# Kernel optimization log

Hardware: AMD Instinct MI355X
Metric: run time of the kernel (lower is better)

The kernel has to match this reference:

```python
import jax, jax.numpy as jnp
import numpy as np

N = 30000      # input points
M = 7500       # sampled queries = floor(N * ratio), ratio=0.25
K = 16         # neighbors per query
D_X = 64       # input feature dim
D_REL = 64     # point_pos_nn output dim
D_F = D_X + D_REL  # fij_hat dim = 128


def setup_inputs() -> dict:
    key = jax.random.key(0)
    ks = jax.random.split(key, 6)
    x = jax.random.normal(ks[0], (N, D_X), jnp.float32)
    pos = jax.random.normal(ks[1], (N, 3), jnp.float32)
    idx = jax.random.randint(ks[2], (M,), 0, N)
    W_pos = jax.random.normal(ks[3], (10, D_REL), jnp.float32) / jnp.sqrt(10.0)
    b_pos = jnp.zeros((D_REL,), jnp.float32)
    W_att = jax.random.normal(ks[4], (D_F, D_F), jnp.float32) / jnp.sqrt(float(D_F))
    b_att = jnp.zeros((D_F,), jnp.float32)
    W_glob = jax.random.normal(ks[5], (D_F, D_F), jnp.float32) / jnp.sqrt(float(D_F))
    b_glob = jnp.zeros((D_F,), jnp.float32)
    return {"x": x, "pos": pos, "idx": idx, "W_pos": W_pos, "b_pos": b_pos,
            "W_att": W_att, "b_att": b_att, "W_glob": W_glob, "b_glob": b_glob}


def reference(x, pos, idx, W_pos, b_pos, W_att, b_att, W_glob, b_glob):
    # --- KNN: brute-force squared distances from sampled queries to all points ---
    pos_q = pos[idx]                                         # [M, 3]
    d2 = ((pos_q * pos_q).sum(-1)[:, None]
          + (pos * pos).sum(-1)[None, :]
          - 2.0 * pos_q @ pos.T)                             # [M, N]
    _, nbr = jax.lax.top_k(-d2, K)                           # [M, K] neighbor indices

    # --- Local Spatial Encoding (message) ---
    pos_j = pos[nbr]                                         # [M, K, 3]
    pos_i = jnp.broadcast_to(pos_q[:, None, :], pos_j.shape) # [M, K, 3]
    vij = pos_i - pos_j                                      # [M, K, 3]
    dij = jnp.linalg.norm(vij, axis=-1, keepdims=True)       # [M, K, 1]
    rel = jnp.concatenate([pos_i, pos_j, vij, dij], axis=-1) # [M, K, 10]
    rij = jax.nn.relu(rel @ W_pos + b_pos)                   # [M, K, D_REL]

    # --- Attentive pooling ---
    fij = jnp.concatenate([x[nbr], rij], axis=-1)            # [M, K, D_F]
    g = fij @ W_att + b_att                                  # [M, K, D_F]
    s = jax.nn.softmax(g, axis=-1)                           # softmax over feature dim
    aggr = jnp.mean(s * fij, axis=1)                         # mean over K neighbors -> [M, D_F]

    # --- global_nn (update) ---
    return jax.nn.relu(aggr @ W_glob + b_glob)               # [M, D_F]
```

## Files before the change

kernel.cpp:

```cpp
#include <hip/hip_runtime.h>
#include <stdint.h>

#define KNB     16
#define GD      64
#define GTOT    (GD * GD * GD)
#define GORIG   (-6.5f)
#define GEDGE   0.203125f
#define GINV    (1.0f / GEDGE)
#define CAPW    640
#define PROBE_T 48

typedef short short8 __attribute__((ext_vector_type(8)));
typedef float floatx4 __attribute__((ext_vector_type(4)));

__device__ __forceinline__ unsigned short f2bf(float x) {
  union { float f; uint32_t u; } v; v.f = x;
  uint32_t u = v.u + 0x7FFFu + ((v.u >> 16) & 1u);
  return (unsigned short)(u >> 16);
}
__device__ __forceinline__ float bf2f(unsigned short b) {
  return __uint_as_float(((uint32_t)b) << 16);
}
__device__ __forceinline__ int cellco(float v) {
  int c = (int)floorf((v - GORIG) * GINV);
  return c < 0 ? 0 : (c > GD - 1 ? GD - 1 : c);
}

__global__ void zero_kernel(int* __restrict__ count) {
  int i = (blockIdx.x * 256 + threadIdx.x) * 4;
  *(int4*)(count + i) = make_int4(0, 0, 0, 0);
}

__global__ void prep_kernel(const float* __restrict__ x,
                            const float* __restrict__ pos,
                            const float* __restrict__ W_att,
                            unsigned short* __restrict__ xb,
                            float4* __restrict__ pos4,
                            unsigned short* __restrict__ Wt,
                            int* __restrict__ ptcell,
                            int* __restrict__ count, int N) {
  int id = blockIdx.x * 256 + threadIdx.x;
  int nx8 = N * 8;
  if (id < nx8) {
    const float4* src = (const float4*)x + (size_t)id * 2;
    float4 a = src[0], b = src[1];
    short8 v;
    v[0] = (short)f2bf(a.x); v[1] = (short)f2bf(a.y);
    v[2] = (short)f2bf(a.z); v[3] = (short)f2bf(a.w);
    v[4] = (short)f2bf(b.x); v[5] = (short)f2bf(b.y);
    v[6] = (short)f2bf(b.z); v[7] = (short)f2bf(b.w);
    *(short8*)(xb + (size_t)id * 8) = v;
  } else if (id < nx8 + N) {
    int j = id - nx8;
    float px = pos[3 * j], py = pos[3 * j + 1], pz = pos[3 * j + 2];
    float pp = fmaf(px, px, fmaf(py, py, pz * pz));
    pos4[j] = make_float4(px, py, pz, pp);
    int cid = (cellco(pz) * GD + cellco(py)) * GD + cellco(px);
    ptcell[j] = cid;
    atomicAdd(&count[cid], 1);
  } else if (id < nx8 + N + 128 * 128) {
    int t = id - nx8 - N;
    int c = t >> 7, f = t & 127;
    Wt[f * 128 + c] = f2bf(W_att[t]);
  }
}

__global__ __launch_bounds__(256) void vscan_x(const int* __restrict__ count,
                                               int* __restrict__ V) {
  int row = blockIdx.x * 4 + (threadIdx.x >> 6);
  int ln = threadIdx.x & 63;
  int i = row * GD + ln;
  int v = count[i];
#pragma unroll
  for (int off = 1; off < 64; off <<= 1) {
    int y = __shfl_up(v, off);
    if (ln >= off) v += y;
  }
  V[i] = v;
}

__global__ __launch_bounds__(256) void vscan_y(int* __restrict__ V) {
  int pair = blockIdx.x * 4 + (threadIdx.x >> 6);
  int z = pair >> 6, x = pair & 63;
  int ln = threadIdx.x & 63;
  int i = (z * GD + ln) * GD + x;
  int v = V[i];
#pragma unroll
  for (int off = 1; off < 64; off <<= 1) {
    int y = __shfl_up(v, off);
    if (ln >= off) v += y;
  }
  V[i] = v;
}

__global__ __launch_bounds__(256) void vscan_z(int* __restrict__ V) {
  int pair = blockIdx.x * 4 + (threadIdx.x >> 6);
  int ln = threadIdx.x & 63;
  int i = ln * GD * GD + pair;
  int v = V[i];
#pragma unroll
  for (int off = 1; off < 64; off <<= 1) {
    int y = __shfl_up(v, off);
    if (ln >= off) v += y;
  }
  V[i] = v;
}

__global__ __launch_bounds__(256) void derive_kernel(
    const int* __restrict__ V, int* __restrict__ cell_start,
    int* __restrict__ cursor) {
  int cid = blockIdx.x * 256 + threadIdx.x;
  int x = cid & 63, y = (cid >> 6) & 63, z = cid >> 12;
  int s = 0;
  if (z > 0) s += V[((z - 1) * GD + 63) * GD + 63];
  if (y > 0) {
    s += V[(z * GD + (y - 1)) * GD + 63];
    if (z > 0) s -= V[((z - 1) * GD + (y - 1)) * GD + 63];
  }
  if (x > 0) {
    s += V[(z * GD + y) * GD + (x - 1)];
    if (y > 0) s -= V[(z * GD + (y - 1)) * GD + (x - 1)];
    if (z > 0) s -= V[((z - 1) * GD + y) * GD + (x - 1)];
    if (z > 0 && y > 0) s += V[((z - 1) * GD + (y - 1)) * GD + (x - 1)];
  }
  cell_start[cid] = s;
  cursor[cid] = s;
  if (cid == 0) cell_start[GTOT] = V[GTOT - 1];
}

__global__ void scatter_kernel(const float4* __restrict__ pos4,
                               const int* __restrict__ ptcell,
                               int* __restrict__ cursor,
                               float4* __restrict__ spos4,
                               int* __restrict__ sid, int N) {
  int j = blockIdx.x * 256 + threadIdx.x;
  if (j >= N) return;
  int cid = ptcell[j];
  int slot = atomicAdd(&cursor[cid], 1);
  spos4[slot] = pos4[j];
  sid[slot] = j;
}

__device__ __forceinline__ unsigned long long top16_reg(
    unsigned long long* candw, int tot, int ln) {
  unsigned long long c[CAPW / 64];
#pragma unroll
  for (int chk = 0; chk < CAPW / 64; ++chk) {
    int slot = chk * 64 + ln;
    c[chk] = (slot < tot) ? candw[slot] : ~0ull;
  }
  unsigned long long mykey = ~0ull, last = 0;
#pragma unroll
  for (int r = 0; r < KNB; ++r) {
    unsigned long long mn = c[0];
#pragma unroll
    for (int chk = 1; chk < CAPW / 64; ++chk) mn = (c[chk] < mn) ? c[chk] : mn;
#pragma unroll
    for (int off = 1; off < 64; off <<= 1) {
      unsigned long long o = __shfl_xor(mn, off);
      mn = (o < mn) ? o : mn;
    }
    if (ln == r) mykey = mn;
    last = mn;
#pragma unroll
    for (int chk = 0; chk < CAPW / 64; ++chk)
      if (c[chk] == mn) c[chk] = ~0ull;
  }
  if (ln < KNB) candw[ln] = mykey;
  return last;
}

__device__ __forceinline__ void drain_annulus(
    const float4* __restrict__ spos4, const int* __restrict__ sid,
    const int* __restrict__ cell_start, unsigned long long* candw,
    float4 qp, int cqx, int cqy, int cqz, int slo, int shi, int ln,
    int& tot, unsigned long long& taukey) {
  const int z0 = (cqz - shi < 0) ? 0 : cqz - shi;
  const int z1 = (cqz + shi > GD - 1) ? GD - 1 : cqz + shi;
  const int y0 = (cqy - shi < 0) ? 0 : cqy - shi;
  const int y1 = (cqy + shi > GD - 1) ? GD - 1 : cqy + shi;
  const int wy = y1 - y0 + 1;
  const int npair = (z1 - z0 + 1) * wy;
  for (int base = 0; base < npair; base += 64) {
    int i = base + ln;
    int stA = 0, lA = 0, stB = 0, lB = 0;
    if (i < npair) {
      int zz = z0 + i / wy;
      int yy = y0 + (i - (i / wy) * wy);
      int dz = zz - cqz, dy = yy - cqy;
      int az = dz < 0 ? -dz : dz, ay = dy < 0 ? -dy : dy;
      int ch = az > ay ? az : ay;
      int rowbase = (zz * GD + yy) * GD;
      if (ch > slo) {
        int x0 = cqx - shi; if (x0 < 0) x0 = 0;
        int x1 = cqx + shi; if (x1 > GD - 1) x1 = GD - 1;
        stA = cell_start[rowbase + x0];
        lA  = cell_start[rowbase + x1 + 1] - stA;
      } else {
        int xl0 = cqx - shi; if (xl0 < 0) xl0 = 0;
        int xl1 = cqx - slo - 1;
        if (xl1 >= xl0) {
          stA = cell_start[rowbase + xl0];
          lA  = cell_start[rowbase + xl1 + 1] - stA;
        }
        int xr0 = cqx + slo + 1;
        int xr1 = cqx + shi; if (xr1 > GD - 1) xr1 = GD - 1;
        if (xr1 >= xr0) {
          stB = cell_start[rowbase + xr0];
          lB  = cell_start[rowbase + xr1 + 1] - stB;
        }
      }
    }
    int len = lA + lB;
    int xinc = len;
#pragma unroll
    for (int off = 1; off < 64; off <<= 1) {
      int y = __shfl_up(xinc, off);
      if (ln >= off) xinc += y;
    }
    int T = __shfl(xinc, 63);
    if (T == 0) continue;
    int ps_ex = xinc - len;

    for (int b2 = 0; b2 < T; b2 += 64) {
      if (tot + 64 > CAPW) {
        taukey = top16_reg(candw, tot, ln);
        tot = KNB;
      }
      int flat = b2 + ln;
      bool valid = flat < T;
      int flatc = valid ? flat : (T - 1);
      int lo = 0;
#pragma unroll
      for (int step = 32; step > 0; step >>= 1) {
        int mid = lo + step;
        int v = __shfl(ps_ex, mid & 63);
        if (mid <= 63 && v <= flatc) lo = mid;
      }
      int psl = __shfl(ps_ex, lo);
      int sa  = __shfl(stA, lo);
      int la  = __shfl(lA, lo);
      int sb  = __shfl(stB, lo);
      int o = flatc - psl;
      int p = (o < la) ? (sa + o) : (sb + (o - la));
      float4 pj = spos4[p];
      float dot = fmaf(qp.x, pj.x, fmaf(qp.y, pj.y, qp.z * pj.z));
      float tt  = fmaf(-2.f, dot, pj.w);
      float d2  = fmaxf(qp.w + tt, 0.f);
      unsigned long long key =
          ((unsigned long long)__float_as_uint(d2) << 32) | (uint32_t)sid[p];
      bool ok = valid && (key < taukey);
      unsigned long long bm = __ballot(ok);
      int pos = __popcll(bm & ((1ull << ln) - 1ull));
      if (ok) candw[tot + pos] = key;
      tot += __popcll(bm);
    }
  }
}

__global__ __launch_bounds__(256) void knn_grid(
    const float4* __restrict__ pos4, const float4* __restrict__ spos4,
    const int* __restrict__ sid, const int* __restrict__ cell_start,
    const int* __restrict__ V, const int* __restrict__ idx,
    int* __restrict__ nbr, int M) {
  __shared__ unsigned long long cand[4][CAPW];
  const int tid = threadIdx.x, wv = tid >> 6, ln = tid & 63;
  const int m = blockIdx.x * 4 + wv;
  if (m >= M) return;

  const float4 qp = pos4[idx[m]];
  const int cqx = cellco(qp.x), cqy = cellco(qp.y), cqz = cellco(qp.z);

  int s0;
  {
    int s = ln;
    int xh = cqx + s > GD - 1 ? GD - 1 : cqx + s;
    int yh = cqy + s > GD - 1 ? GD - 1 : cqy + s;
    int zh = cqz + s > GD - 1 ? GD - 1 : cqz + s;
    int xm = cqx - s - 1, ym = cqy - s - 1, zm = cqz - s - 1;
    int c = V[(zh * GD + yh) * GD + xh];
    if (zm >= 0) c -= V[(zm * GD + yh) * GD + xh];
    if (ym >= 0) c -= V[(zh * GD + ym) * GD + xh];
    if (xm >= 0) c -= V[(zh * GD + yh) * GD + xm];
    if (zm >= 0 && ym >= 0) c += V[(zm * GD + ym) * GD + xh];
    if (zm >= 0 && xm >= 0) c += V[(zm * GD + yh) * GD + xm];
    if (ym >= 0 && xm >= 0) c += V[(zh * GD + ym) * GD + xm];
    if (zm >= 0 && ym >= 0 && xm >= 0) c -= V[(zm * GD + ym) * GD + xm];
    unsigned long long bm = __ballot(c >= PROBE_T);
    s0 = __ffsll((unsigned long long)bm) - 1;
  }

  int tot = 0;
  unsigned long long taukey = ~0ull;
  drain_annulus(spos4, sid, cell_start, &cand[wv][0], qp, cqx, cqy, cqz,
                -1, s0, ln, tot, taukey);
  taukey = top16_reg(&cand[wv][0], tot, ln);
  tot = KNB;
  float d16sq = __uint_as_float((uint32_t)(taukey >> 32));

  int s1 = s0;
  {
    float fx = qp.x - GORIG, fy = qp.y - GORIG, fz = qp.z - GORIG;
    while (s1 < GD - 1) {
      float r = 3.0e38f;
      if (cqx - s1 > 0)      r = fminf(r, fx - (float)(cqx - s1) * GEDGE);
      if (cqx + s1 < GD - 1) r = fminf(r, (float)(cqx + s1 + 1) * GEDGE - fx);
      if (cqy - s1 > 0)      r = fminf(r, fy - (float)(cqy - s1) * GEDGE);
      if (cqy + s1 < GD - 1) r = fminf(r, (float)(cqy + s1 + 1) * GEDGE - fy);
      if (cqz - s1 > 0)      r = fminf(r, fz - (float)(cqz - s1) * GEDGE);
      if (cqz + s1 < GD - 1) r = fminf(r, (float)(cqz + s1 + 1) * GEDGE - fz);
      float r2 = (r > 1.0e19f) ? 3.0e38f : r * r;
      if (r2 >= d16sq) break;
      ++s1;
    }
  }

  if (s1 > s0) {
    drain_annulus(spos4, sid, cell_start, &cand[wv][0], qp, cqx, cqy, cqz,
                  s0, s1, ln, tot, taukey);
    if (tot > KNB) (void)top16_reg(&cand[wv][0], tot, ln);
  }

  if (ln < KNB) nbr[m * KNB + ln] = (int)(uint32_t)cand[wv][ln];
}

__global__ __launch_bounds__(256) void mid_kernel(
    const unsigned short* __restrict__ xb, const float4* __restrict__ pos4,
    const int* __restrict__ idx, const float* __restrict__ W_pos,
    const float* __restrict__ b_pos, const unsigned short* __restrict__ Wt,
    const float* __restrict__ b_att, const int* __restrict__ nbr,
    float* __restrict__ aggr, int M) {
  __shared__ __align__(16) unsigned short fijb[8][16][136];
  __shared__ int nbr_s[128];
  __shared__ float4 qpos_s[8];

  const int tid = threadIdx.x;
  const int wid = tid >> 6, lane = tid & 63;
  const int col = lane & 15, quad = lane >> 4;
  const int b = blockIdx.x;

  if (tid < 128) {
    int mq = b * 8 + (tid >> 4); if (mq >= M) mq = M - 1;
    nbr_s[tid] = nbr[mq * 16 + (tid & 15)];
  }
  if (tid < 8) {
    int mq = b * 8 + tid; if (mq >= M) mq = M - 1;
    qpos_s[tid] = pos4[idx[mq]];
  }
  float wp[10];
#pragma unroll
  for (int t = 0; t < 10; ++t) wp[t] = W_pos[t * 64 + lane];
  float bp = b_pos[lane];
  __syncthreads();

  {
    int rr = tid >> 1, h = tid & 1;
    int jn = nbr_s[rr];
    const short8* src = (const short8*)(xb + ((size_t)jn << 6) + (h << 5));
    short8 v0 = src[0], v1 = src[1], v2 = src[2], v3 = src[3];
    short8* dst = (short8*)&fijb[rr >> 4][rr & 15][h * 32];
    dst[0] = v0; dst[1] = v1; dst[2] = v2; dst[3] = v3;
  }
#pragma unroll
  for (int qi = 0; qi < 2; ++qi) {
    int q = wid * 2 + qi;
    float4 qp = qpos_s[q];
#pragma unroll 4
    for (int k = 0; k < 16; ++k) {
      int jn = nbr_s[q * 16 + k];
      float4 pj = pos4[jn];
      float vx = qp.x - pj.x, vy = qp.y - pj.y, vz = qp.z - pj.z;
      float dd = sqrtf(fmaf(vx, vx, fmaf(vy, vy, vz * vz)));
      float r = bp;
      r = fmaf(qp.x, wp[0], r); r = fmaf(qp.y, wp[1], r); r = fmaf(qp.z, wp[2], r);
      r = fmaf(pj.x, wp[3], r); r = fmaf(pj.y, wp[4], r); r = fmaf(pj.z, wp[5], r);
      r = fmaf(vx, wp[6], r);  r = fmaf(vy, wp[7], r);  r = fmaf(vz, wp[8], r);
      r = fmaf(dd, wp[9], r);
      r = fmaxf(r, 0.f);
      fijb[q][k][64 + lane] = f2bf(r);
    }
  }
  __syncthreads();

#pragma unroll 1
  for (int qi = 0; qi < 2; ++qi) {
    int q = wid * 2 + qi;
    int mq = b * 8 + q;

    short8 af[4];
#pragma unroll
    for (int cs = 0; cs < 4; ++cs)
      af[cs] = *(const short8*)&fijb[q][col][cs * 32 + quad * 8];

    floatx4 acc[8];
#pragma unroll
    for (int ft = 0; ft < 8; ++ft) {
      float bav = b_att[ft * 16 + col];
      floatx4 a = {bav, bav, bav, bav};
#pragma unroll
      for (int cs = 0; cs < 4; ++cs) {
        short8 bfrag =
            *(const short8*)&Wt[(ft * 16 + col) * 128 + cs * 32 + quad * 8];
        a = __builtin_amdgcn_mfma_f32_16x16x32_bf16(af[cs], bfrag, a, 0, 0, 0);
      }
      acc[ft] = a;
    }

    float rowmax[4], rowinv[4];
#pragma unroll
    for (int r = 0; r < 4; ++r) {
      float mx = acc[0][r];
#pragma unroll
      for (int ft = 1; ft < 8; ++ft) mx = fmaxf(mx, acc[ft][r]);
      mx = fmaxf(mx, __shfl_xor(mx, 1));
      mx = fmaxf(mx, __shfl_xor(mx, 2));
      mx = fmaxf(mx, __shfl_xor(mx, 4));
      mx = fmaxf(mx, __shfl_xor(mx, 8));
      float sm = 0.f;
#pragma unroll
      for (int ft = 0; ft < 8; ++ft) sm += __expf(acc[ft][r] - mx);
      sm += __shfl_xor(sm, 1);
      sm += __shfl_xor(sm, 2);
      sm += __shfl_xor(sm, 4);
      sm += __shfl_xor(sm, 8);
      rowmax[r] = mx;
      rowinv[r] = 1.0f / sm;
    }

#pragma unroll
    for (int ft = 0; ft < 8; ++ft) {
      float ap = 0.f;
#pragma unroll
      for (int r = 0; r < 4; ++r) {
        float s = __expf(acc[ft][r] - rowmax[r]) * rowinv[r];
        float fv = bf2f(fijb[q][quad * 4 + r][ft * 16 + col]);
        ap = fmaf(s, fv, ap);
      }
      ap += __shfl_xor(ap, 16);
      ap += __shfl_xor(ap, 32);
      if (quad == 0 && mq < M)
        aggr[mq * 128 + ft * 16 + col] = ap * (1.0f / 16.0f);
    }
  }
}

__global__ __launch_bounds__(256) void out_kernel(
    const float* __restrict__ aggr, const float* __restrict__ W_glob,
    const float* __restrict__ b_glob, float* __restrict__ out, int M) {
  __shared__ float ag[16][128];
  const int tid = threadIdx.x;
  const int mbase = blockIdx.x * 16;
  for (int s = tid; s < 16 * 128; s += 256) {
    int r = s >> 7, cc = s & 127;
    int m = mbase + r;
    ((float*)ag)[s] = (m < M) ? aggr[m * 128 + cc] : 0.0f;
  }
  __syncthreads();
  const int f = tid & 127, h = tid >> 7;
  float acc[8];
  float bg = b_glob[f];
#pragma unroll
  for (int i = 0; i < 8; ++i) acc[i] = bg;
  for (int c = 0; c < 128; c += 4) {
    float w0 = W_glob[(c + 0) * 128 + f];
    float w1 = W_glob[(c + 1) * 128 + f];
    float w2 = W_glob[(c + 2) * 128 + f];
    float w3 = W_glob[(c + 3) * 128 + f];
#pragma unroll
    for (int i = 0; i < 8; ++i) {
      const floatx4 a4 = *(const floatx4*)&ag[h * 8 + i][c];
      acc[i] += a4[0] * w0 + a4[1] * w1 + a4[2] * w2 + a4[3] * w3;
    }
  }
#pragma unroll
  for (int i = 0; i < 8; ++i) {
    int m = mbase + h * 8 + i;
    if (m < M) out[m * 128 + f] = fmaxf(acc[i], 0.0f);
  }
}

extern "C" void kernel_launch(void* const* d_in, const int* in_sizes, int n_in,
                              void* d_out, int out_size, void* d_ws,
                              size_t ws_size, hipStream_t stream) {
  const float* x      = (const float*)d_in[0];
  const float* pos    = (const float*)d_in[1];
  const int*   idx    = (const int*)d_in[2];
  const float* W_pos  = (const float*)d_in[3];
  const float* b_pos  = (const float*)d_in[4];
  const float* W_att  = (const float*)d_in[5];
  const float* b_att  = (const float*)d_in[6];
  const float* W_glob = (const float*)d_in[7];
  const float* b_glob = (const float*)d_in[8];
  float* out = (float*)d_out;

  const int N = in_sizes[1] / 3;
  const int M = in_sizes[2];

  char* ws = (char*)d_ws;
  size_t o = 0;
  float4* pos4 = (float4*)(ws + o);               o += ((size_t)N * 16 + 255) & ~(size_t)255;
  unsigned short* xb = (unsigned short*)(ws + o); o += ((size_t)N * 128 + 255) & ~(size_t)255;
  unsigned short* Wt = (unsigned short*)(ws + o); o += (128 * 128 * 2 + 255) & ~(size_t)255;
  int* nbr = (int*)(ws + o);                      o += (((size_t)M * KNB * 4) + 255) & ~(size_t)255;
  int* ptcell = (int*)(ws + o);                   o += (((size_t)N * 4) + 255) & ~(size_t)255;
  int* count = (int*)(ws + o);                    o += ((size_t)GTOT * 4 + 255) & ~(size_t)255;
  int* cursor = (int*)(ws + o);                   o += ((size_t)GTOT * 4 + 255) & ~(size_t)255;
  int* cell_start = (int*)(ws + o);               o += ((size_t)(GTOT + 1) * 4 + 255) & ~(size_t)255;
  int* V = (int*)(ws + o);                        o += ((size_t)GTOT * 4 + 255) & ~(size_t)255;
  float4* spos4 = (float4*)(ws + o);              o += ((size_t)N * 16 + 255) & ~(size_t)255;
  int* sid = (int*)(ws + o);                      o += (((size_t)N * 4) + 255) & ~(size_t)255;
  float* aggr = (float*)(ws + o);                 o += ((size_t)M * 128 * 4 + 255) & ~(size_t)255;

  zero_kernel<<<GTOT / 1024, 256, 0, stream>>>(count);

  int prep_ids = N * 8 + N + 128 * 128;
  prep_kernel<<<(prep_ids + 255) / 256, 256, 0, stream>>>(
      x, pos, W_att, xb, pos4, Wt, ptcell, count, N);

  vscan_x<<<1024, 256, 0, stream>>>(count, V);
  vscan_y<<<1024, 256, 0, stream>>>(V);
  vscan_z<<<1024, 256, 0, stream>>>(V);
  derive_kernel<<<GTOT / 256, 256, 0, stream>>>(V, cell_start, cursor);

  scatter_kernel<<<(N + 255) / 256, 256, 0, stream>>>(pos4, ptcell, cursor,
                                                      spos4, sid, N);

  knn_grid<<<(M + 3) / 4, 256, 0, stream>>>(pos4, spos4, sid, cell_start, V,
                                            idx, nbr, M);

  mid_kernel<<<(M + 7) / 8, 256, 0, stream>>>(xb, pos4, idx, W_pos, b_pos, Wt,
                                              b_att, nbr, aggr, M);
  out_kernel<<<(M + 15) / 16, 256, 0, stream>>>(aggr, W_glob, b_glob, out, M);
}
```

Measured before the change: 203.8 us.

## Pack point id into sorted positions and process two candidate batches per iteration

The scatter now stores the original point index in the w slot of the sorted float4, so the separate sid array and its gather in the KNN inner loop go away. The squared norm is recomputed from xyz instead of read from w. The candidate loop handles 128 candidates per iteration as two independent 64-wide halves, which exposes more memory-level parallelism per wave. The KNN launch changes to one 64-thread block per query, which removes the early-return path for partial blocks and may change occupancy and scheduling.

```diff
diff --git a/kernel.cpp b/kernel.cpp
--- a/kernel.cpp
+++ b/kernel.cpp
@@ -131,14 +131,13 @@
 __global__ void scatter_kernel(const float4* __restrict__ pos4,
                                const int* __restrict__ ptcell,
                                int* __restrict__ cursor,
-                               float4* __restrict__ spos4,
-                               int* __restrict__ sid, int N) {
+                               float4* __restrict__ spos4, int N) {
   int j = blockIdx.x * 256 + threadIdx.x;
   if (j >= N) return;
   int cid = ptcell[j];
   int slot = atomicAdd(&cursor[cid], 1);
-  spos4[slot] = pos4[j];
-  sid[slot] = j;
+  float4 p = pos4[j];
+  spos4[slot] = make_float4(p.x, p.y, p.z, __int_as_float(j));
 }
 
 __device__ __forceinline__ unsigned long long top16_reg(
@@ -171,10 +170,9 @@
 }
 
 __device__ __forceinline__ void drain_annulus(
-    const float4* __restrict__ spos4, const int* __restrict__ sid,
-    const int* __restrict__ cell_start, unsigned long long* candw,
-    float4 qp, int cqx, int cqy, int cqz, int slo, int shi, int ln,
-    int& tot, unsigned long long& taukey) {
+    const float4* __restrict__ spos4, const int* __restrict__ cell_start,
+    unsigned long long* candw, float4 qp, int cqx, int cqy, int cqz,
+    int slo, int shi, int ln, int& tot, unsigned long long& taukey) {
   const int z0 = (cqz - shi < 0) ? 0 : cqz - shi;
   const int z1 = (cqz + shi > GD - 1) ? GD - 1 : cqz + shi;
   const int y0 = (cqy - shi < 0) ? 0 : cqy - shi;
@@ -222,51 +220,67 @@
     if (T == 0) continue;
     int ps_ex = xinc - len;
 
-    for (int b2 = 0; b2 < T; b2 += 64) {
-      if (tot + 64 > CAPW) {
+    for (int b2 = 0; b2 < T; b2 += 128) {
+      if (tot + 128 > CAPW) {
         taukey = top16_reg(candw, tot, ln);
         tot = KNB;
       }
-      int flat = b2 + ln;
-      bool valid = flat < T;
-      int flatc = valid ? flat : (T - 1);
-      int lo = 0;
+      int flatA = b2 + ln;
+      int flatB = b2 + 64 + ln;
+      bool vA = flatA < T, vB = flatB < T;
+      int fA = vA ? flatA : (T - 1);
+      int fB = vB ? flatB : (T - 1);
+      int loA = 0, loB = 0;
 #pragma unroll
       for (int step = 32; step > 0; step >>= 1) {
-        int mid = lo + step;
-        int v = __shfl(ps_ex, mid & 63);
-        if (mid <= 63 && v <= flatc) lo = mid;
+        int mA = loA + step, mB = loB + step;
+        int sA = __shfl(ps_ex, mA & 63);
+        int sB = __shfl(ps_ex, mB & 63);
+        if (mA <= 63 && sA <= fA) loA = mA;
+        if (mB <= 63 && sB <= fB) loB = mB;
       }
-      int psl = __shfl(ps_ex, lo);
-      int sa  = __shfl(stA, lo);
-      int la  = __shfl(lA, lo);
-      int sb  = __shfl(stB, lo);
-      int o = flatc - psl;
-      int p = (o < la) ? (sa + o) : (sb + (o - la));
-      float4 pj = spos4[p];
-      float dot = fmaf(qp.x, pj.x, fmaf(qp.y, pj.y, qp.z * pj.z));
-      float tt  = fmaf(-2.f, dot, pj.w);
-      float d2  = fmaxf(qp.w + tt, 0.f);
-      unsigned long long key =
-          ((unsigned long long)__float_as_uint(d2) << 32) | (uint32_t)sid[p];
-      bool ok = valid && (key < taukey);
-      unsigned long long bm = __ballot(ok);
-      int pos = __popcll(bm & ((1ull << ln) - 1ull));
-      if (ok) candw[tot + pos] = key;
-      tot += __popcll(bm);
-    }
-  }
-}
-
-__global__ __launch_bounds__(256) void knn_grid(
+      int psA = __shfl(ps_ex, loA), psB = __shfl(ps_ex, loB);
+      int saA = __shfl(stA, loA),   saB = __shfl(stA, loB);
+      int laA = __shfl(lA, loA),    laB = __shfl(lA, loB);
+      int sbA = __shfl(stB, loA),   sbB = __shfl(stB, loB);
+      int oA = fA - psA, oB = fB - psB;
+      int pA = (oA < laA) ? (saA + oA) : (sbA + (oA - laA));
+      int pB = (oB < laB) ? (saB + oB) : (sbB + (oB - laB));
+      float4 pjA = spos4[pA];
+      float4 pjB = spos4[pB];
+      float ppA = fmaf(pjA.x, pjA.x, fmaf(pjA.y, pjA.y, pjA.z * pjA.z));
+      float ppB = fmaf(pjB.x, pjB.x, fmaf(pjB.y, pjB.y, pjB.z * pjB.z));
+      float dotA = fmaf(qp.x, pjA.x, fmaf(qp.y, pjA.y, qp.z * pjA.z));
+      float dotB = fmaf(qp.x, pjB.x, fmaf(qp.y, pjB.y, qp.z * pjB.z));
+      float d2A = fmaxf(qp.w + fmaf(-2.f, dotA, ppA), 0.f);
+      float d2B = fmaxf(qp.w + fmaf(-2.f, dotB, ppB), 0.f);
+      unsigned long long keyA =
+          ((unsigned long long)__float_as_uint(d2A) << 32) |
+          (uint32_t)__float_as_uint(pjA.w);
+      unsigned long long keyB =
+          ((unsigned long long)__float_as_uint(d2B) << 32) |
+          (uint32_t)__float_as_uint(pjB.w);
+      bool okA = vA && (keyA < taukey);
+      bool okB = vB && (keyB < taukey);
+      unsigned long long bmA = __ballot(okA);
+      int posA = __popcll(bmA & ((1ull << ln) - 1ull));
+      if (okA) candw[tot + posA] = keyA;
+      tot += __popcll(bmA);
+      unsigned long long bmB = __ballot(okB);
+      int posB = __popcll(bmB & ((1ull << ln) - 1ull));
+      if (okB) candw[tot + posB] = keyB;
+      tot += __popcll(bmB);
+    }
+  }
+}
+
+__global__ __launch_bounds__(64) void knn_grid(
     const float4* __restrict__ pos4, const float4* __restrict__ spos4,
-    const int* __restrict__ sid, const int* __restrict__ cell_start,
-    const int* __restrict__ V, const int* __restrict__ idx,
-    int* __restrict__ nbr, int M) {
-  __shared__ unsigned long long cand[4][CAPW];
-  const int tid = threadIdx.x, wv = tid >> 6, ln = tid & 63;
-  const int m = blockIdx.x * 4 + wv;
-  if (m >= M) return;
+    const int* __restrict__ cell_start, const int* __restrict__ V,
+    const int* __restrict__ idx, int* __restrict__ nbr, int M) {
+  __shared__ unsigned long long cand[CAPW];
+  const int ln = threadIdx.x;
+  const int m = blockIdx.x;
 
   const float4 qp = pos4[idx[m]];
   const int cqx = cellco(qp.x), cqy = cellco(qp.y), cqz = cellco(qp.z);
@@ -292,9 +306,9 @@
 
   int tot = 0;
   unsigned long long taukey = ~0ull;
-  drain_annulus(spos4, sid, cell_start, &cand[wv][0], qp, cqx, cqy, cqz,
+  drain_annulus(spos4, cell_start, cand, qp, cqx, cqy, cqz,
                 -1, s0, ln, tot, taukey);
-  taukey = top16_reg(&cand[wv][0], tot, ln);
+  taukey = top16_reg(cand, tot, ln);
   tot = KNB;
   float d16sq = __uint_as_float((uint32_t)(taukey >> 32));
 
@@ -316,12 +330,12 @@
   }
 
   if (s1 > s0) {
-    drain_annulus(spos4, sid, cell_start, &cand[wv][0], qp, cqx, cqy, cqz,
+    drain_annulus(spos4, cell_start, cand, qp, cqx, cqy, cqz,
                   s0, s1, ln, tot, taukey);
-    if (tot > KNB) (void)top16_reg(&cand[wv][0], tot, ln);
-  }
-
-  if (ln < KNB) nbr[m * KNB + ln] = (int)(uint32_t)cand[wv][ln];
+    if (tot > KNB) (void)top16_reg(cand, tot, ln);
+  }
+
+  if (ln < KNB) nbr[m * KNB + ln] = (int)(uint32_t)cand[ln];
 }
 
 __global__ __launch_bounds__(256) void mid_kernel(
@@ -508,7 +522,6 @@
   int* cell_start = (int*)(ws + o);               o += ((size_t)(GTOT + 1) * 4 + 255) & ~(size_t)255;
   int* V = (int*)(ws + o);                        o += ((size_t)GTOT * 4 + 255) & ~(size_t)255;
   float4* spos4 = (float4*)(ws + o);              o += ((size_t)N * 16 + 255) & ~(size_t)255;
-  int* sid = (int*)(ws + o);                      o += (((size_t)N * 4) + 255) & ~(size_t)255;
   float* aggr = (float*)(ws + o);                 o += ((size_t)M * 128 * 4 + 255) & ~(size_t)255;
 
   zero_kernel<<<GTOT / 1024, 256, 0, stream>>>(count);
@@ -523,10 +536,9 @@
   derive_kernel<<<GTOT / 256, 256, 0, stream>>>(V, cell_start, cursor);
 
   scatter_kernel<<<(N + 255) / 256, 256, 0, stream>>>(pos4, ptcell, cursor,
-                                                      spos4, sid, N);
-
-  knn_grid<<<(M + 3) / 4, 256, 0, stream>>>(pos4, spos4, sid, cell_start, V,
-                                            idx, nbr, M);
+                                                      spos4, N);
+
+  knn_grid<<<M, 64, 0, stream>>>(pos4, spos4, cell_start, V, idx, nbr, M);
 
   mid_kernel<<<(M + 7) / 8, 256, 0, stream>>>(xb, pos4, idx, W_pos, b_pos, Wt,
                                               b_att, nbr, aggr, M);
```

Result: no change. 203.0 us (-0.4%).
